# Kernel optimization log

Hardware: AMD Instinct MI355X
Metric: run time of the kernel (lower is better)

Reference implementation:

```python
import jax, jax.numpy as jnp
import numpy as np
from jax import lax

B, S, V, E, H = 64, 512, 50000, 300, 256


def _run_lstm(x, w_ih, w_hh, b_ih, b_hh, reverse):
    # x: [B,S,D]; w_ih: [4H,D]; w_hh: [4H,H]. PyTorch gate order: i,f,g,o.
    gx = jnp.einsum('bsd,gd->sbg', x, w_ih) + b_ih + b_hh  # [S,B,4H]
    Hh = w_hh.shape[1]

    def step(carry, g):
        h, c = carry
        g = g + h @ w_hh.T
        i, f, gg, o = jnp.split(g, 4, axis=-1)
        c = jax.nn.sigmoid(f) * c + jax.nn.sigmoid(i) * jnp.tanh(gg)
        h = jax.nn.sigmoid(o) * jnp.tanh(c)
        return (h, c), h

    init = (jnp.zeros((x.shape[0], Hh), x.dtype), jnp.zeros((x.shape[0], Hh), x.dtype))
    _, hs = lax.scan(step, init, gx, reverse=reverse)  # outputs aligned to input time order
    return jnp.swapaxes(hs, 0, 1)  # [B,S,H]


def _bilstm(x, wif, whf, bif, bhf, wib, whb, bib, bhb):
    fwd = _run_lstm(x, wif, whf, bif, bhf, False)
    bwd = _run_lstm(x, wib, whb, bib, bhb, True)
    return jnp.concatenate([fwd, bwd], axis=-1)  # [B,S,2H]


def setup_inputs() -> dict:
    key = jax.random.key(0)
    ks = iter(jax.random.split(key, 32))
    k = 1.0 / np.sqrt(H)
    u = lambda shape: jax.random.uniform(next(ks), shape, jnp.float32, -k, k)
    inp = {
        'input_ids': jax.random.randint(next(ks), (B, S), 0, V),
        'labels': jax.random.uniform(next(ks), (B, S), jnp.float32),
        'input_masks': jnp.ones((B, S), jnp.int64),
        'emb': jax.random.normal(next(ks), (V, E), jnp.float32) * 0.1,
    }
    # layer 0 (input E), layer 1 (input 2H); forward and backward directions
    for layer, d_in in ((0, E), (1, 2 * H)):
        for direc in ('f', 'b'):
            inp[f'w_ih_l{layer}{direc}'] = u((4 * H, d_in))
            inp[f'w_hh_l{layer}{direc}'] = u((4 * H, H))
            inp[f'b_ih_l{layer}{direc}'] = u((4 * H,))
            inp[f'b_hh_l{layer}{direc}'] = u((4 * H,))
    inp['w_lin'] = u((H,))
    inp['b_lin'] = u(())
    return inp


def reference(input_ids, labels, input_masks, emb,
              w_ih_l0f, w_hh_l0f, b_ih_l0f, b_hh_l0f,
              w_ih_l0b, w_hh_l0b, b_ih_l0b, b_hh_l0b,
              w_ih_l1f, w_hh_l1f, b_ih_l1f, b_hh_l1f,
              w_ih_l1b, w_hh_l1b, b_ih_l1b, b_hh_l1b,
              w_lin, b_lin):
    x = emb[input_ids]  # one-shot gather, replaces the double python loop: [B,S,E]
    h1 = _bilstm(x, w_ih_l0f, w_hh_l0f, b_ih_l0f, b_hh_l0f,
                 w_ih_l0b, w_hh_l0b, b_ih_l0b, b_hh_l0b)
    h2 = _bilstm(h1, w_ih_l1f, w_hh_l1f, b_ih_l1f, b_hh_l1f,
                 w_ih_l1b, w_hh_l1b, b_ih_l1b, b_hh_l1b)  # [B,S,2H]
    b, s = h2.shape[0], h2.shape[1]
    mean_dir = h2.reshape(b, s, 2, H).mean(axis=2)  # mean over directions
    scores = jax.nn.sigmoid(jnp.einsum('bsh,h->bs', mean_dir, w_lin) + b_lin)
    mask = input_masks.astype(scores.dtype)
    err = (scores - labels) ** 2 * mask
    loss = jnp.mean(jnp.sum(err, axis=1) / jnp.sum(mask, axis=1))
    return scores, loss
```

## Files before the change

### kernel.cpp

```cpp
#include <hip/hip_runtime.h>
#include <hip/hip_bf16.h>
#include <stdint.h>

#define B_  64
#define S_  512
#define E_  300
#define H_  256
#define T_  (B_*S_)
#define G4H 1024

using half8  = __attribute__((ext_vector_type(8))) _Float16;
using half4  = __attribute__((ext_vector_type(4))) _Float16;
using float4v = __attribute__((ext_vector_type(4))) float;

union H2 { _Float16 h[2]; uint32_t u; };

__device__ inline float sigm(float x) { return 1.f / (1.f + __expf(-x)); }
__device__ inline float tanhf_(float x) {
  float cx = fminf(fmaxf(x, -15.f), 15.f);
  float e = __expf(2.f * cx);
  return (e - 1.f) / (e + 1.f);
}

#define BARRIER() asm volatile("s_waitcnt lgkmcnt(0)\n\ts_barrier" ::: "memory")

__device__ inline void ld3_dev(const uint64_t* p0, const uint64_t* p1,
                               const uint64_t* p2, uint4& a, uint4& b, uint4& c) {
  asm volatile(
      "global_load_dwordx4 %0, %3, off sc0 sc1\n\t"
      "global_load_dwordx4 %1, %4, off sc0 sc1\n\t"
      "global_load_dwordx4 %2, %5, off sc0 sc1\n\t"
      "s_waitcnt vmcnt(0)"
      : "=&v"(a), "=&v"(b), "=&v"(c)
      : "v"(p0), "v"(p1), "v"(p2) : "memory");
}
__device__ inline uint4 ldx4_pin(const _Float16* p) {
  uint4 r;
  asm volatile("global_load_dwordx4 %0, %1, off\n\ts_waitcnt vmcnt(0)"
               : "=v"(r) : "v"(p));
  return r;
}

__global__ __launch_bounds__(256) void k_prep_wih(const float* __restrict__ wf,
    const float* __restrict__ wb, _Float16* __restrict__ Bt,
    int KIN, int KP, int total)
{
  int idx = blockIdx.x * 256 + threadIdx.x;
  if (idx >= total) return;
  int n = idx / KP, k = idx % KP;
  int dd = n >> 10, nn = n & 1023;
  int row = (nn & 3) * 256 + (nn >> 2);
  const float* src = dd ? wb : wf;
  Bt[idx] = (_Float16)(k < KIN ? src[row * KIN + k] : 0.f);
}

__global__ __launch_bounds__(256) void k_prep_whh(const float* __restrict__ wf,
    const float* __restrict__ wb, _Float16* __restrict__ Wr)
{
  int idx = blockIdx.x * 256 + threadIdx.x;
  int dd = idx >> 18;
  int rem = idx & 262143;
  int n = rem >> 8, k = rem & 255;
  int row = (n & 3) * 256 + (n >> 2);
  Wr[idx] = (_Float16)((dd ? wb : wf)[row * 256 + k]);
}

__global__ void k_prep_bias(const float* __restrict__ bif, const float* __restrict__ bhf,
    const float* __restrict__ bib, const float* __restrict__ bhb, float* __restrict__ bias)
{
  int n = blockIdx.x * 256 + threadIdx.x;
  int dd = n >> 10, nn = n & 1023;
  int row = (nn & 3) * 256 + (nn >> 2);
  bias[n] = dd ? (bib[row] + bhb[row]) : (bif[row] + bhf[row]);
}

__global__ __launch_bounds__(256) void k_gather(const int* __restrict__ ids,
    const float* __restrict__ emb, _Float16* __restrict__ xbf)
{
  int idx = blockIdx.x * 256 + threadIdx.x;
  int tt = idx / 40;
  int ch = idx % 40;
  int b = tt & 63, s = tt >> 6;
  int id = ids[b * S_ + s];
  const float* src = emb + (size_t)id * E_ + ch * 8;
  half8 v;
#pragma unroll
  for (int e = 0; e < 8; ++e) {
    int k = ch * 8 + e;
    v[e] = (_Float16)(k < E_ ? src[e] : 0.f);
  }
  *(half8*)(xbf + (size_t)tt * 320 + ch * 8) = v;
}

template<int K>
__global__ __launch_bounds__(256) void k_gemm(const _Float16* __restrict__ A,
    const _Float16* __restrict__ Bt, const float* __restrict__ bias,
    _Float16* __restrict__ gx)
{
  __shared__ _Float16 sA[128 * 72];
  __shared__ _Float16 sB[128 * 72];
  const int tid = threadIdx.x;
  const int t0 = blockIdx.y * 128;
  const int n0 = blockIdx.x * 128;
  const int lane = tid & 63, wid = tid >> 6;
  const int l15 = lane & 15, q = lane >> 4;
  const int wm = wid & 1, wn = wid >> 1;

  float4v acc[4][4] = {};

  for (int kt = 0; kt < K / 64; ++kt) {
    __syncthreads();
#pragma unroll
    for (int c = 0; c < 4; ++c) {
      int f = tid * 4 + c;
      int row = f >> 3, seg = f & 7;
      *(half8*)&sA[row * 72 + seg * 8] =
          *(const half8*)(A + (size_t)(t0 + row) * K + kt * 64 + seg * 8);
      *(half8*)&sB[row * 72 + seg * 8] =
          *(const half8*)(Bt + (size_t)(n0 + row) * K + kt * 64 + seg * 8);
    }
    __syncthreads();
#pragma unroll
    for (int kk = 0; kk < 2; ++kk) {
      half8 a[4], b[4];
#pragma unroll
      for (int mt = 0; mt < 4; ++mt)
        a[mt] = *(const half8*)&sA[(wm * 64 + mt * 16 + l15) * 72 + kk * 32 + q * 8];
#pragma unroll
      for (int nt = 0; nt < 4; ++nt)
        b[nt] = *(const half8*)&sB[(wn * 64 + nt * 16 + l15) * 72 + kk * 32 + q * 8];
#pragma unroll
      for (int mt = 0; mt < 4; ++mt)
#pragma unroll
        for (int nt = 0; nt < 4; ++nt)
          acc[mt][nt] = __builtin_amdgcn_mfma_f32_16x16x32_f16(a[mt], b[nt], acc[mt][nt], 0, 0, 0);
    }
  }

#pragma unroll
  for (int mt = 0; mt < 4; ++mt) {
#pragma unroll
    for (int nt = 0; nt < 4; ++nt) {
      int token = t0 + wm * 64 + mt * 16 + q * 4;
      int n = n0 + wn * 64 + nt * 16 + l15;
      float bs = bias[n];
      size_t base = (size_t)(n >> 10) * ((size_t)T_ * G4H) + (size_t)token * G4H + (n & 1023);
#pragma unroll
      for (int r = 0; r < 4; ++r)
        gx[base + (size_t)r * G4H] = (_Float16)(acc[mt][nt][r] + bs);
    }
  }
}

template<int LAYER>
__global__ __launch_bounds__(256, 1) void k_rec(const _Float16* __restrict__ gx,
    const _Float16* __restrict__ Wr, uint64_t* __restrict__ hx,
    _Float16* __restrict__ h1bf, float* __restrict__ pd2,
    const float* __restrict__ w_lin)
{
  const int tid = threadIdx.x;
  const int role = blockIdx.x;
  const int cg = role >> 2, rg = role & 3;
  const int d = cg >> 2, g = cg & 3;
  const int lane = tid & 63, wv = tid >> 6;
  const int l15 = lane & 15, q = lane >> 4;
  const int b0g = g * 16;
  const int n0g = rg * 256;

  __shared__ _Float16 hstage[16 * 288];
  __shared__ float    preS[16 * 260];

  for (int i = tid; i < 16 * 144; i += 256)
    ((uint32_t*)hstage)[i] = 0u;

  uint4 wreg[4][8];
#pragma unroll
  for (int nt = 0; nt < 4; ++nt)
#pragma unroll
    for (int kt = 0; kt < 8; ++kt)
      wreg[nt][kt] = ldx4_pin(Wr +
          (size_t)(d * G4H + n0g + wv * 64 + nt * 16 + l15) * H_ + kt * 32 + q * 8);

  const int bl = tid >> 4;
  const int jl4 = (tid & 15) * 4;
  const int bglob = b0g + bl;
  const int jg = rg * 64 + jl4;
  float wl[4];
#pragma unroll
  for (int cc = 0; cc < 4; ++cc) wl[cc] = w_lin[jg + cc];
  float creg[4] = {0.f, 0.f, 0.f, 0.f};

  uint64_t* base = hx + (size_t)cg * 2 * 2048;
  const int off2 = tid * 2;
  const int q2a = (rg + 1) & 3, q2b = (rg + 2) & 3, q2c = (rg + 3) & 3;

  half8 gxa, gxb;
  {
    const int time0 = d ? (S_ - 1) : 0;
    const _Float16* gp = gx + ((size_t)d * T_ + (size_t)time0 * B_ + bglob) * G4H
                           + n0g + (tid & 15) * 16;
    gxa = *(const half8*)(gp);
    gxb = *(const half8*)(gp + 8);
  }

  for (int t = 0; t < S_; ++t) {
    const int time = d ? (S_ - 1 - t) : t;

    if (t > 0) {
      const uint64_t* ss = base + (size_t)(t & 1) * 2048;
      const uint32_t tt = (uint32_t)t;
      uint32_t dat[6];
      unsigned pend = 0x3fu;
      for (;;) {
        uint4 A, Bv, C;
        ld3_dev(ss + q2a * 512 + off2, ss + q2b * 512 + off2,
                ss + q2c * 512 + off2, A, Bv, C);
        if ((pend & 1u)  && A.y  == tt) { dat[0] = A.x;  pend &= ~1u; }
        if ((pend & 2u)  && A.w  == tt) { dat[1] = A.z;  pend &= ~2u; }
        if ((pend & 4u)  && Bv.y == tt) { dat[2] = Bv.x; pend &= ~4u; }
        if ((pend & 8u)  && Bv.w == tt) { dat[3] = Bv.z; pend &= ~8u; }
        if ((pend & 16u) && C.y  == tt) { dat[4] = C.x;  pend &= ~16u; }
        if ((pend & 32u) && C.w  == tt) { dat[5] = C.z;  pend &= ~32u; }
        if (!pend) break;
      }
      const int sb = tid >> 4, jp = (tid & 15) * 2;
      uint2 va; va.x = dat[0]; va.y = dat[1];
      uint2 vb; vb.x = dat[2]; vb.y = dat[3];
      uint2 vc; vc.x = dat[4]; vc.y = dat[5];
      *(uint2*)&((uint32_t*)hstage)[sb * 144 + q2a * 32 + jp] = va;
      *(uint2*)&((uint32_t*)hstage)[sb * 144 + q2b * 32 + jp] = vb;
      *(uint2*)&((uint32_t*)hstage)[sb * 144 + q2c * 32 + jp] = vc;
    }
    BARRIER();

    half8 gxa_n, gxb_n;
    {
      const int tn = (t + 1 < S_) ? t + 1 : t;
      const int timen = d ? (S_ - 1 - tn) : tn;
      const _Float16* gp = gx + ((size_t)d * T_ + (size_t)timen * B_ + bglob) * G4H
                             + n0g + (tid & 15) * 16;
      gxa_n = *(const half8*)(gp);
      gxb_n = *(const half8*)(gp + 8);
    }

    float4v acc[4] = {};
#pragma unroll
    for (int kt = 0; kt < 8; ++kt) {
      half8 a = *(const half8*)&hstage[l15 * 288 + kt * 32 + q * 8];
#pragma unroll
      for (int nt = 0; nt < 4; ++nt)
        acc[nt] = __builtin_amdgcn_mfma_f32_16x16x32_f16(
            a, __builtin_bit_cast(half8, wreg[nt][kt]), acc[nt], 0, 0, 0);
    }
#pragma unroll
    for (int nt = 0; nt < 4; ++nt)
#pragma unroll
      for (int r = 0; r < 4; ++r)
        preS[(q * 4 + r) * 260 + wv * 64 + nt * 16 + l15] = acc[nt][r];
    BARRIER();

    half4 hv4;
    float partial = 0.f;
#pragma unroll
    for (int cc = 0; cc < 4; ++cc) {
      float4v p = *(const float4v*)&preS[bl * 260 + (jl4 + cc) * 4];
      float gxi = (float)(cc < 2 ? gxa[cc * 4 + 0] : gxb[(cc - 2) * 4 + 0]);
      float gxf = (float)(cc < 2 ? gxa[cc * 4 + 1] : gxb[(cc - 2) * 4 + 1]);
      float gxg = (float)(cc < 2 ? gxa[cc * 4 + 2] : gxb[(cc - 2) * 4 + 2]);
      float gxo = (float)(cc < 2 ? gxa[cc * 4 + 3] : gxb[(cc - 2) * 4 + 3]);
      float gi = p[0] + gxi, gf = p[1] + gxf, gg = p[2] + gxg, go = p[3] + gxo;
      float cv = sigm(gf) * creg[cc] + sigm(gi) * tanhf_(gg);
      float hv = sigm(go) * tanhf_(cv);
      creg[cc] = cv;
      hv4[cc] = (_Float16)hv;
      if (LAYER == 1) partial += 0.5f * hv * wl[cc];
    }

    {
      H2 p0; p0.h[0] = hv4[0]; p0.h[1] = hv4[1];
      H2 p1; p1.h[0] = hv4[2]; p1.h[1] = hv4[3];
      uint32_t tg = (uint32_t)(t + 1);
      uint64_t w0 = ((uint64_t)tg << 32) | p0.u;
      uint64_t w1 = ((uint64_t)tg << 32) | p1.u;
      uint64_t* sd = base + (size_t)((t + 1) & 1) * 2048 + rg * 512 + off2;
      __hip_atomic_store(sd + 0, w0, __ATOMIC_RELAXED, __HIP_MEMORY_SCOPE_AGENT);
      __hip_atomic_store(sd + 1, w1, __ATOMIC_RELAXED, __HIP_MEMORY_SCOPE_AGENT);
    }

    *(half4*)&hstage[bl * 288 + jg] = hv4;

    if (LAYER == 0) {
      *(half4*)(h1bf + ((size_t)time * B_ + bglob) * 512 + d * H_ + jg) = hv4;
    } else {
      partial += __shfl_xor(partial, 1);
      partial += __shfl_xor(partial, 2);
      partial += __shfl_xor(partial, 4);
      partial += __shfl_xor(partial, 8);
      if ((tid & 15) == 0)
        atomicAdd(pd2 + ((size_t)d * B_ + bglob) * S_ + time, partial);
    }

    gxa = gxa_n; gxb = gxb_n;
  }
}

__global__ __launch_bounds__(256) void k_final(const float* __restrict__ pd2,
    const float* __restrict__ labels, const int* __restrict__ masks,
    const float* __restrict__ b_lin, float* __restrict__ out)
{
  int b = blockIdx.x;
  int tid = threadIdx.x;
  float bl = b_lin[0];
  float se = 0.f, sm = 0.f;
  for (int s = tid; s < S_; s += 256) {
    float p = pd2[(size_t)b * S_ + s] + pd2[(size_t)(B_ + b) * S_ + s];
    float sc = sigm(p + bl);
    out[b * S_ + s] = sc;
    float m = (float)masks[b * S_ + s];
    float e = sc - labels[b * S_ + s];
    se += e * e * m;
    sm += m;
  }
  for (int off = 1; off < 64; off <<= 1) {
    se += __shfl_xor(se, off);
    sm += __shfl_xor(sm, off);
  }
  __shared__ float rs[4], rm[4];
  int wid = tid >> 6;
  if ((tid & 63) == 0) { rs[wid] = se; rm[wid] = sm; }
  __syncthreads();
  if (tid == 0) {
    float te = 0.f, tm = 0.f;
    for (int w = 0; w < 4; ++w) { te += rs[w]; tm += rm[w]; }
    atomicAdd(out + T_, (te / tm) * (1.f / 64.f));
  }
}

extern "C" void kernel_launch(void* const* d_in, const int* in_sizes, int n_in,
                              void* d_out, int out_size, void* d_ws, size_t ws_size,
                              hipStream_t stream)
{
  (void)in_sizes; (void)n_in; (void)out_size; (void)ws_size;
  const int*   ids    = (const int*)d_in[0];
  const float* labels = (const float*)d_in[1];
  const int*   masks  = (const int*)d_in[2];
  const float* emb    = (const float*)d_in[3];
  const float* w_ih_0f = (const float*)d_in[4];
  const float* w_hh_0f = (const float*)d_in[5];
  const float* b_ih_0f = (const float*)d_in[6];
  const float* b_hh_0f = (const float*)d_in[7];
  const float* w_ih_0b = (const float*)d_in[8];
  const float* w_hh_0b = (const float*)d_in[9];
  const float* b_ih_0b = (const float*)d_in[10];
  const float* b_hh_0b = (const float*)d_in[11];
  const float* w_ih_1f = (const float*)d_in[12];
  const float* w_hh_1f = (const float*)d_in[13];
  const float* b_ih_1f = (const float*)d_in[14];
  const float* b_hh_1f = (const float*)d_in[15];
  const float* w_ih_1b = (const float*)d_in[16];
  const float* w_hh_1b = (const float*)d_in[17];
  const float* b_ih_1b = (const float*)d_in[18];
  const float* b_hh_1b = (const float*)d_in[19];
  const float* w_lin   = (const float*)d_in[20];
  const float* b_lin   = (const float*)d_in[21];
  float* out = (float*)d_out;

  char* ws = (char*)d_ws;
  size_t off = 0;
  auto alloc = [&](size_t bytes) -> char* {
    char* p = ws + off;
    off += (bytes + 255) & ~(size_t)255;
    return p;
  };
  _Float16* xbf   = (_Float16*)alloc((size_t)T_ * 320 * 2);
  _Float16* h1bf  = (_Float16*)alloc((size_t)T_ * 512 * 2);
  _Float16* gx    = (_Float16*)alloc((size_t)2 * T_ * G4H * 2);
  _Float16* Bt0   = (_Float16*)alloc((size_t)2048 * 320 * 2);
  _Float16* Bt1   = (_Float16*)alloc((size_t)2048 * 512 * 2);
  _Float16* Wr0   = (_Float16*)alloc((size_t)2 * G4H * H_ * 2);
  _Float16* Wr1   = (_Float16*)alloc((size_t)2 * G4H * H_ * 2);
  float*    bias0 = (float*)alloc(2048 * 4);
  float*    bias1 = (float*)alloc(2048 * 4);
  uint64_t* hx0   = (uint64_t*)alloc((size_t)8 * 2 * 2048 * 8);
  uint64_t* hx1   = (uint64_t*)alloc((size_t)8 * 2 * 2048 * 8);
  float*    pd2   = (float*)alloc((size_t)2 * B_ * S_ * 4);

  k_prep_wih<<<(2048 * 320) / 256, 256, 0, stream>>>(w_ih_0f, w_ih_0b, Bt0, 300, 320, 2048 * 320);
  k_prep_wih<<<(2048 * 512) / 256, 256, 0, stream>>>(w_ih_1f, w_ih_1b, Bt1, 512, 512, 2048 * 512);
  k_prep_whh<<<524288 / 256, 256, 0, stream>>>(w_hh_0f, w_hh_0b, Wr0);
  k_prep_whh<<<524288 / 256, 256, 0, stream>>>(w_hh_1f, w_hh_1b, Wr1);
  k_prep_bias<<<8, 256, 0, stream>>>(b_ih_0f, b_hh_0f, b_ih_0b, b_hh_0b, bias0);
  k_prep_bias<<<8, 256, 0, stream>>>(b_ih_1f, b_hh_1f, b_ih_1b, b_hh_1b, bias1);
  k_gather<<<(T_ * 40) / 256, 256, 0, stream>>>(ids, emb, xbf);

  hipMemsetAsync(hx0, 0, (size_t)8 * 2 * 2048 * 8, stream);
  hipMemsetAsync(hx1, 0, (size_t)8 * 2 * 2048 * 8, stream);
  hipMemsetAsync(pd2, 0, (size_t)2 * B_ * S_ * 4, stream);
  hipMemsetAsync((char*)d_out + (size_t)T_ * 4, 0, 4, stream);

  k_gemm<320><<<dim3(16, 256), 256, 0, stream>>>(xbf, Bt0, bias0, gx);
  k_rec<0><<<32, 256, 0, stream>>>(gx, Wr0, hx0, h1bf, pd2, w_lin);

  k_gemm<512><<<dim3(16, 256), 256, 0, stream>>>(h1bf, Bt1, bias1, gx);
  k_rec<1><<<32, 256, 0, stream>>>(gx, Wr1, hx1, h1bf, pd2, w_lin);

  k_final<<<64, 256, 0, stream>>>(pd2, labels, masks, b_lin, out);
}
```

Measured before the change: 2.846 ms.

## Run each LSTM recurrence group in one workgroup, dropping cross-block global handoff

The recurrent kernel now gives each (direction, batch-group) to a single 512-thread workgroup instead of four 256-thread workgroups that exchanged hidden-state slices through tagged global-memory polling every step. W_hh is split between registers (6 of 8 tiles) and swizzled LDS (2 tiles), and h is double-buffered in LDS so each step needs one barrier. The gx pre-activation is loaded straight into the MFMA accumulators, and gates are computed directly from the accumulators, removing the preS staging. This removes the per-step inter-CU spin-wait latency, but leaves only 8 workgroups running, each doing four times the MFMA work per step with heavy register and LDS use.

```diff
diff --git a/kernel.cpp b/kernel.cpp
--- a/kernel.cpp
+++ b/kernel.cpp
@@ -13,8 +13,6 @@
 using half4  = __attribute__((ext_vector_type(4))) _Float16;
 using float4v = __attribute__((ext_vector_type(4))) float;
 
-union H2 { _Float16 h[2]; uint32_t u; };
-
 __device__ inline float sigm(float x) { return 1.f / (1.f + __expf(-x)); }
 __device__ inline float tanhf_(float x) {
   float cx = fminf(fmaxf(x, -15.f), 15.f);
@@ -24,16 +22,6 @@
 
 #define BARRIER() asm volatile("s_waitcnt lgkmcnt(0)\n\ts_barrier" ::: "memory")
 
-__device__ inline void ld3_dev(const uint64_t* p0, const uint64_t* p1,
-                               const uint64_t* p2, uint4& a, uint4& b, uint4& c) {
-  asm volatile(
-      "global_load_dwordx4 %0, %3, off sc0 sc1\n\t"
-      "global_load_dwordx4 %1, %4, off sc0 sc1\n\t"
-      "global_load_dwordx4 %2, %5, off sc0 sc1\n\t"
-      "s_waitcnt vmcnt(0)"
-      : "=&v"(a), "=&v"(b), "=&v"(c)
-      : "v"(p0), "v"(p1), "v"(p2) : "memory");
-}
 __device__ inline uint4 ldx4_pin(const _Float16* p) {
   uint4 r;
   asm volatile("global_load_dwordx4 %0, %1, off\n\ts_waitcnt vmcnt(0)"
@@ -153,154 +141,118 @@
 }
 
 template<int LAYER>
-__global__ __launch_bounds__(256, 1) void k_rec(const _Float16* __restrict__ gx,
-    const _Float16* __restrict__ Wr, uint64_t* __restrict__ hx,
-    _Float16* __restrict__ h1bf, float* __restrict__ pd2,
-    const float* __restrict__ w_lin)
-{
+__global__ __launch_bounds__(512, 2) void k_rec(const _Float16* __restrict__ gx,
+    const _Float16* __restrict__ Wr, _Float16* __restrict__ h1bf,
+    float* __restrict__ pd2, const float* __restrict__ w_lin)
+{
+  extern __shared__ char smem[];
+  _Float16* wlds = (_Float16*)smem;
+  _Float16* hst  = (_Float16*)(smem + 131072);
+  float*    wls  = (float*)(smem + 131072 + 18432);
+
   const int tid = threadIdx.x;
-  const int role = blockIdx.x;
-  const int cg = role >> 2, rg = role & 3;
+  const int cg = blockIdx.x;
   const int d = cg >> 2, g = cg & 3;
-  const int lane = tid & 63, wv = tid >> 6;
+  const int wv = tid >> 6, lane = tid & 63;
   const int l15 = lane & 15, q = lane >> 4;
   const int b0g = g * 16;
-  const int n0g = rg * 256;
-
-  __shared__ _Float16 hstage[16 * 288];
-  __shared__ float    preS[16 * 260];
-
-  for (int i = tid; i < 16 * 144; i += 256)
-    ((uint32_t*)hstage)[i] = 0u;
-
-  uint4 wreg[4][8];
-#pragma unroll
-  for (int nt = 0; nt < 4; ++nt)
+  const int bglob = b0g + l15;
+
+  if (tid < 256) wls[tid] = w_lin[tid];
+  for (int i = tid; i < 2 * 16 * 144; i += 512)
+    ((uint32_t*)hst)[i] = 0u;
+
+  uint4 wreg[6][8];
+#pragma unroll
+  for (int nt = 0; nt < 6; ++nt)
 #pragma unroll
     for (int kt = 0; kt < 8; ++kt)
       wreg[nt][kt] = ldx4_pin(Wr +
-          (size_t)(d * G4H + n0g + wv * 64 + nt * 16 + l15) * H_ + kt * 32 + q * 8);
-
-  const int bl = tid >> 4;
-  const int jl4 = (tid & 15) * 4;
-  const int bglob = b0g + bl;
-  const int jg = rg * 64 + jl4;
-  float wl[4];
-#pragma unroll
-  for (int cc = 0; cc < 4; ++cc) wl[cc] = w_lin[jg + cc];
-  float creg[4] = {0.f, 0.f, 0.f, 0.f};
-
-  uint64_t* base = hx + (size_t)cg * 2 * 2048;
-  const int off2 = tid * 2;
-  const int q2a = (rg + 1) & 3, q2b = (rg + 2) & 3, q2c = (rg + 3) & 3;
-
-  half8 gxa, gxb;
+          (size_t)(d * G4H + wv * 128 + nt * 16 + l15) * H_ + kt * 32 + q * 8);
+
+#pragma unroll
+  for (int tt = 0; tt < 2; ++tt)
+#pragma unroll
+    for (int j = 0; j < 8; ++j) {
+      int row = wv * 128 + (6 + tt) * 16 + l15;
+      uint4 w = *(const uint4*)(Wr + (size_t)(d * G4H + row) * H_ + q * 64 + j * 8);
+      int byo = (q * 128 + j * 16) ^ ((l15 & 7) << 4);
+      *(uint4*)(wlds + wv * 8192 + tt * 4096 + l15 * 256 + (byo >> 1)) = w;
+    }
+
+  float creg[8] = {};
+  uint2 gq[8];
+
   {
     const int time0 = d ? (S_ - 1) : 0;
     const _Float16* gp = gx + ((size_t)d * T_ + (size_t)time0 * B_ + bglob) * G4H
-                           + n0g + (tid & 15) * 16;
-    gxa = *(const half8*)(gp);
-    gxb = *(const half8*)(gp + 8);
-  }
+                           + wv * 128 + q * 4;
+#pragma unroll
+    for (int nt = 0; nt < 8; ++nt)
+      gq[nt] = *(const uint2*)(gp + nt * 16);
+  }
+  __syncthreads();
 
   for (int t = 0; t < S_; ++t) {
     const int time = d ? (S_ - 1 - t) : t;
-
-    if (t > 0) {
-      const uint64_t* ss = base + (size_t)(t & 1) * 2048;
-      const uint32_t tt = (uint32_t)t;
-      uint32_t dat[6];
-      unsigned pend = 0x3fu;
-      for (;;) {
-        uint4 A, Bv, C;
-        ld3_dev(ss + q2a * 512 + off2, ss + q2b * 512 + off2,
-                ss + q2c * 512 + off2, A, Bv, C);
-        if ((pend & 1u)  && A.y  == tt) { dat[0] = A.x;  pend &= ~1u; }
-        if ((pend & 2u)  && A.w  == tt) { dat[1] = A.z;  pend &= ~2u; }
-        if ((pend & 4u)  && Bv.y == tt) { dat[2] = Bv.x; pend &= ~4u; }
-        if ((pend & 8u)  && Bv.w == tt) { dat[3] = Bv.z; pend &= ~8u; }
-        if ((pend & 16u) && C.y  == tt) { dat[4] = C.x;  pend &= ~16u; }
-        if ((pend & 32u) && C.w  == tt) { dat[5] = C.z;  pend &= ~32u; }
-        if (!pend) break;
-      }
-      const int sb = tid >> 4, jp = (tid & 15) * 2;
-      uint2 va; va.x = dat[0]; va.y = dat[1];
-      uint2 vb; vb.x = dat[2]; vb.y = dat[3];
-      uint2 vc; vc.x = dat[4]; vc.y = dat[5];
-      *(uint2*)&((uint32_t*)hstage)[sb * 144 + q2a * 32 + jp] = va;
-      *(uint2*)&((uint32_t*)hstage)[sb * 144 + q2b * 32 + jp] = vb;
-      *(uint2*)&((uint32_t*)hstage)[sb * 144 + q2c * 32 + jp] = vc;
-    }
-    BARRIER();
-
-    half8 gxa_n, gxb_n;
+    const int cur = t & 1, nxt = cur ^ 1;
+
+    float4v acc[8];
+#pragma unroll
+    for (int nt = 0; nt < 8; ++nt) {
+      half4 hz = __builtin_bit_cast(half4, gq[nt]);
+      acc[nt][0] = (float)hz[0];
+      acc[nt][1] = (float)hz[1];
+      acc[nt][2] = (float)hz[2];
+      acc[nt][3] = (float)hz[3];
+    }
+
     {
       const int tn = (t + 1 < S_) ? t + 1 : t;
       const int timen = d ? (S_ - 1 - tn) : tn;
       const _Float16* gp = gx + ((size_t)d * T_ + (size_t)timen * B_ + bglob) * G4H
-                             + n0g + (tid & 15) * 16;
-      gxa_n = *(const half8*)(gp);
-      gxb_n = *(const half8*)(gp + 8);
-    }
-
-    float4v acc[4] = {};
+                             + wv * 128 + q * 4;
+#pragma unroll
+      for (int nt = 0; nt < 8; ++nt)
+        gq[nt] = *(const uint2*)(gp + nt * 16);
+    }
+
 #pragma unroll
     for (int kt = 0; kt < 8; ++kt) {
-      half8 a = *(const half8*)&hstage[l15 * 288 + kt * 32 + q * 8];
-#pragma unroll
-      for (int nt = 0; nt < 4; ++nt)
+      half8 hf = *(const half8*)(hst + cur * 4608 + l15 * 288 + kt * 32 + q * 8);
+      int byr = (kt * 64 + q * 16) ^ ((l15 & 7) << 4);
+      half8 w6 = *(const half8*)(wlds + wv * 8192 + l15 * 256 + (byr >> 1));
+      half8 w7 = *(const half8*)(wlds + wv * 8192 + 4096 + l15 * 256 + (byr >> 1));
+#pragma unroll
+      for (int nt = 0; nt < 6; ++nt)
         acc[nt] = __builtin_amdgcn_mfma_f32_16x16x32_f16(
-            a, __builtin_bit_cast(half8, wreg[nt][kt]), acc[nt], 0, 0, 0);
-    }
-#pragma unroll
-    for (int nt = 0; nt < 4; ++nt)
-#pragma unroll
-      for (int r = 0; r < 4; ++r)
-        preS[(q * 4 + r) * 260 + wv * 64 + nt * 16 + l15] = acc[nt][r];
+            __builtin_bit_cast(half8, wreg[nt][kt]), hf, acc[nt], 0, 0, 0);
+      acc[6] = __builtin_amdgcn_mfma_f32_16x16x32_f16(w6, hf, acc[6], 0, 0, 0);
+      acc[7] = __builtin_amdgcn_mfma_f32_16x16x32_f16(w7, hf, acc[7], 0, 0, 0);
+    }
+
+    float partial = 0.f;
+#pragma unroll
+    for (int nt = 0; nt < 8; ++nt) {
+      const int cell = wv * 32 + nt * 4 + q;
+      float cv = sigm(acc[nt][1]) * creg[nt] + sigm(acc[nt][0]) * tanhf_(acc[nt][2]);
+      float hv = sigm(acc[nt][3]) * tanhf_(cv);
+      creg[nt] = cv;
+      _Float16 hf16 = (_Float16)hv;
+      hst[nxt * 4608 + l15 * 288 + cell] = hf16;
+      if (LAYER == 0)
+        h1bf[((size_t)time * B_ + bglob) * 512 + d * H_ + cell] = hf16;
+      else
+        partial += 0.5f * hv * wls[cell];
+    }
+    if (LAYER == 1) {
+      partial += __shfl_xor(partial, 16);
+      partial += __shfl_xor(partial, 32);
+      if (q == 0)
+        atomicAdd(pd2 + ((size_t)d * B_ + bglob) * S_ + time, partial);
+    }
+
     BARRIER();
-
-    half4 hv4;
-    float partial = 0.f;
-#pragma unroll
-    for (int cc = 0; cc < 4; ++cc) {
-      float4v p = *(const float4v*)&preS[bl * 260 + (jl4 + cc) * 4];
-      float gxi = (float)(cc < 2 ? gxa[cc * 4 + 0] : gxb[(cc - 2) * 4 + 0]);
-      float gxf = (float)(cc < 2 ? gxa[cc * 4 + 1] : gxb[(cc - 2) * 4 + 1]);
-      float gxg = (float)(cc < 2 ? gxa[cc * 4 + 2] : gxb[(cc - 2) * 4 + 2]);
-      float gxo = (float)(cc < 2 ? gxa[cc * 4 + 3] : gxb[(cc - 2) * 4 + 3]);
-      float gi = p[0] + gxi, gf = p[1] + gxf, gg = p[2] + gxg, go = p[3] + gxo;
-      float cv = sigm(gf) * creg[cc] + sigm(gi) * tanhf_(gg);
-      float hv = sigm(go) * tanhf_(cv);
-      creg[cc] = cv;
-      hv4[cc] = (_Float16)hv;
-      if (LAYER == 1) partial += 0.5f * hv * wl[cc];
-    }
-
-    {
-      H2 p0; p0.h[0] = hv4[0]; p0.h[1] = hv4[1];
-      H2 p1; p1.h[0] = hv4[2]; p1.h[1] = hv4[3];
-      uint32_t tg = (uint32_t)(t + 1);
-      uint64_t w0 = ((uint64_t)tg << 32) | p0.u;
-      uint64_t w1 = ((uint64_t)tg << 32) | p1.u;
-      uint64_t* sd = base + (size_t)((t + 1) & 1) * 2048 + rg * 512 + off2;
-      __hip_atomic_store(sd + 0, w0, __ATOMIC_RELAXED, __HIP_MEMORY_SCOPE_AGENT);
-      __hip_atomic_store(sd + 1, w1, __ATOMIC_RELAXED, __HIP_MEMORY_SCOPE_AGENT);
-    }
-
-    *(half4*)&hstage[bl * 288 + jg] = hv4;
-
-    if (LAYER == 0) {
-      *(half4*)(h1bf + ((size_t)time * B_ + bglob) * 512 + d * H_ + jg) = hv4;
-    } else {
-      partial += __shfl_xor(partial, 1);
-      partial += __shfl_xor(partial, 2);
-      partial += __shfl_xor(partial, 4);
-      partial += __shfl_xor(partial, 8);
-      if ((tid & 15) == 0)
-        atomicAdd(pd2 + ((size_t)d * B_ + bglob) * S_ + time, partial);
-    }
-
-    gxa = gxa_n; gxb = gxb_n;
   }
 }
 
@@ -381,9 +333,12 @@
   _Float16* Wr1   = (_Float16*)alloc((size_t)2 * G4H * H_ * 2);
   float*    bias0 = (float*)alloc(2048 * 4);
   float*    bias1 = (float*)alloc(2048 * 4);
-  uint64_t* hx0   = (uint64_t*)alloc((size_t)8 * 2 * 2048 * 8);
-  uint64_t* hx1   = (uint64_t*)alloc((size_t)8 * 2 * 2048 * 8);
   float*    pd2   = (float*)alloc((size_t)2 * B_ * S_ * 4);
+
+  (void)hipFuncSetAttribute(reinterpret_cast<const void*>(&k_rec<0>),
+                            hipFuncAttributeMaxDynamicSharedMemorySize, 150528);
+  (void)hipFuncSetAttribute(reinterpret_cast<const void*>(&k_rec<1>),
+                            hipFuncAttributeMaxDynamicSharedMemorySize, 150528);
 
   k_prep_wih<<<(2048 * 320) / 256, 256, 0, stream>>>(w_ih_0f, w_ih_0b, Bt0, 300, 320, 2048 * 320);
   k_prep_wih<<<(2048 * 512) / 256, 256, 0, stream>>>(w_ih_1f, w_ih_1b, Bt1, 512, 512, 2048 * 512);
@@ -393,16 +348,14 @@
   k_prep_bias<<<8, 256, 0, stream>>>(b_ih_1f, b_hh_1f, b_ih_1b, b_hh_1b, bias1);
   k_gather<<<(T_ * 40) / 256, 256, 0, stream>>>(ids, emb, xbf);
 
-  hipMemsetAsync(hx0, 0, (size_t)8 * 2 * 2048 * 8, stream);
-  hipMemsetAsync(hx1, 0, (size_t)8 * 2 * 2048 * 8, stream);
   hipMemsetAsync(pd2, 0, (size_t)2 * B_ * S_ * 4, stream);
   hipMemsetAsync((char*)d_out + (size_t)T_ * 4, 0, 4, stream);
 
   k_gemm<320><<<dim3(16, 256), 256, 0, stream>>>(xbf, Bt0, bias0, gx);
-  k_rec<0><<<32, 256, 0, stream>>>(gx, Wr0, hx0, h1bf, pd2, w_lin);
+  k_rec<0><<<8, 512, 150528, stream>>>(gx, Wr0, h1bf, pd2, w_lin);
 
   k_gemm<512><<<dim3(16, 256), 256, 0, stream>>>(h1bf, Bt1, bias1, gx);
-  k_rec<1><<<32, 256, 0, stream>>>(gx, Wr1, hx1, h1bf, pd2, w_lin);
+  k_rec<1><<<8, 512, 150528, stream>>>(gx, Wr1, h1bf, pd2, w_lin);
 
   k_final<<<64, 256, 0, stream>>>(pd2, labels, masks, b_lin, out);
 }
```

Measured after the change: 5.567 ms. +95.6%, slower.

## Compute LSTM gates in MFMA registers, removing preactivation LDS round-trip and barrier

Applied to the files above, without the earlier changes.

The recurrent kernel permutes the weight rows held in registers and swaps the MFMA operands, so each lane's accumulator holds the i,f,g,o preactivations for its own hidden units. The gate nonlinearities can then run directly from registers, which drops the preS shared-memory staging and one block barrier per timestep. The accumulator is seeded from the precomputed input projection, the h staging buffer is double-buffered, and w_lin moves to shared memory. The handoff layout between blocks changes to match the new lane mapping, so any mismatch in the permutation would corrupt results.

```diff
diff --git a/kernel.cpp b/kernel.cpp
--- a/kernel.cpp
+++ b/kernel.cpp
@@ -158,53 +158,50 @@
     _Float16* __restrict__ h1bf, float* __restrict__ pd2,
     const float* __restrict__ w_lin)
 {
+  __shared__ _Float16 hst[2][16 * 264];
+  __shared__ float    wls[256];
+
   const int tid = threadIdx.x;
   const int role = blockIdx.x;
   const int cg = role >> 2, rg = role & 3;
   const int d = cg >> 2, g = cg & 3;
   const int lane = tid & 63, wv = tid >> 6;
   const int l15 = lane & 15, q = lane >> 4;
-  const int b0g = g * 16;
-  const int n0g = rg * 256;
-
-  __shared__ _Float16 hstage[16 * 288];
-  __shared__ float    preS[16 * 260];
-
-  for (int i = tid; i < 16 * 144; i += 256)
-    ((uint32_t*)hstage)[i] = 0u;
+  const int bglob = g * 16 + l15;
+
+  if (tid < 256) wls[tid] = w_lin[tid];
+  for (int i = tid; i < 2 * 16 * 132; i += 256)
+    ((uint32_t*)&hst[0][0])[i] = 0u;
 
   uint4 wreg[4][8];
 #pragma unroll
   for (int nt = 0; nt < 4; ++nt)
 #pragma unroll
-    for (int kt = 0; kt < 8; ++kt)
-      wreg[nt][kt] = ldx4_pin(Wr +
-          (size_t)(d * G4H + n0g + wv * 64 + nt * 16 + l15) * H_ + kt * 32 + q * 8);
-
-  const int bl = tid >> 4;
-  const int jl4 = (tid & 15) * 4;
-  const int bglob = b0g + bl;
-  const int jg = rg * 64 + jl4;
-  float wl[4];
-#pragma unroll
-  for (int cc = 0; cc < 4; ++cc) wl[cc] = w_lin[jg + cc];
+    for (int kt = 0; kt < 8; ++kt) {
+      int row = rg * 256 + wv * 64 + (l15 >> 2) * 16 + nt * 4 + (l15 & 3);
+      wreg[nt][kt] = ldx4_pin(Wr + (size_t)(d * G4H + row) * H_ + kt * 32 + q * 8);
+    }
+
   float creg[4] = {0.f, 0.f, 0.f, 0.f};
 
   uint64_t* base = hx + (size_t)cg * 2 * 2048;
   const int off2 = tid * 2;
   const int q2a = (rg + 1) & 3, q2b = (rg + 2) & 3, q2c = (rg + 3) & 3;
-
-  half8 gxa, gxb;
+  const int jloc = rg * 64 + wv * 16 + q * 4;
+
+  uint4 gqa, gqb;
   {
     const int time0 = d ? (S_ - 1) : 0;
     const _Float16* gp = gx + ((size_t)d * T_ + (size_t)time0 * B_ + bglob) * G4H
-                           + n0g + (tid & 15) * 16;
-    gxa = *(const half8*)(gp);
-    gxb = *(const half8*)(gp + 8);
-  }
+                           + rg * 256 + wv * 64 + q * 16;
+    gqa = *(const uint4*)(gp);
+    gqb = *(const uint4*)(gp + 8);
+  }
+  __syncthreads();
 
   for (int t = 0; t < S_; ++t) {
     const int time = d ? (S_ - 1 - t) : t;
+    const int cur = t & 1, nxt = cur ^ 1;
 
     if (t > 0) {
       const uint64_t* ss = base + (size_t)(t & 1) * 2048;
@@ -224,56 +221,57 @@
         if (!pend) break;
       }
       const int sb = tid >> 4, jp = (tid & 15) * 2;
+      uint32_t* hc = (uint32_t*)&hst[cur][0];
       uint2 va; va.x = dat[0]; va.y = dat[1];
       uint2 vb; vb.x = dat[2]; vb.y = dat[3];
       uint2 vc; vc.x = dat[4]; vc.y = dat[5];
-      *(uint2*)&((uint32_t*)hstage)[sb * 144 + q2a * 32 + jp] = va;
-      *(uint2*)&((uint32_t*)hstage)[sb * 144 + q2b * 32 + jp] = vb;
-      *(uint2*)&((uint32_t*)hstage)[sb * 144 + q2c * 32 + jp] = vc;
+      *(uint2*)&hc[sb * 132 + q2a * 32 + jp] = va;
+      *(uint2*)&hc[sb * 132 + q2b * 32 + jp] = vb;
+      *(uint2*)&hc[sb * 132 + q2c * 32 + jp] = vc;
     }
     BARRIER();
 
-    half8 gxa_n, gxb_n;
+    uint4 gqa_n, gqb_n;
     {
       const int tn = (t + 1 < S_) ? t + 1 : t;
       const int timen = d ? (S_ - 1 - tn) : tn;
       const _Float16* gp = gx + ((size_t)d * T_ + (size_t)timen * B_ + bglob) * G4H
-                             + n0g + (tid & 15) * 16;
-      gxa_n = *(const half8*)(gp);
-      gxb_n = *(const half8*)(gp + 8);
-    }
-
-    float4v acc[4] = {};
+                             + rg * 256 + wv * 64 + q * 16;
+      gqa_n = *(const uint4*)(gp);
+      gqb_n = *(const uint4*)(gp + 8);
+    }
+
+    float4v acc[4];
+    {
+      half8 ga = __builtin_bit_cast(half8, gqa);
+      half8 gb = __builtin_bit_cast(half8, gqb);
+#pragma unroll
+      for (int r = 0; r < 4; ++r) {
+        acc[0][r] = (float)ga[r];
+        acc[1][r] = (float)ga[4 + r];
+        acc[2][r] = (float)gb[r];
+        acc[3][r] = (float)gb[4 + r];
+      }
+    }
+
 #pragma unroll
     for (int kt = 0; kt < 8; ++kt) {
-      half8 a = *(const half8*)&hstage[l15 * 288 + kt * 32 + q * 8];
+      half8 hf = *(const half8*)&hst[cur][l15 * 264 + kt * 32 + q * 8];
 #pragma unroll
       for (int nt = 0; nt < 4; ++nt)
         acc[nt] = __builtin_amdgcn_mfma_f32_16x16x32_f16(
-            a, __builtin_bit_cast(half8, wreg[nt][kt]), acc[nt], 0, 0, 0);
-    }
-#pragma unroll
-    for (int nt = 0; nt < 4; ++nt)
-#pragma unroll
-      for (int r = 0; r < 4; ++r)
-        preS[(q * 4 + r) * 260 + wv * 64 + nt * 16 + l15] = acc[nt][r];
-    BARRIER();
+            __builtin_bit_cast(half8, wreg[nt][kt]), hf, acc[nt], 0, 0, 0);
+    }
 
     half4 hv4;
     float partial = 0.f;
 #pragma unroll
-    for (int cc = 0; cc < 4; ++cc) {
-      float4v p = *(const float4v*)&preS[bl * 260 + (jl4 + cc) * 4];
-      float gxi = (float)(cc < 2 ? gxa[cc * 4 + 0] : gxb[(cc - 2) * 4 + 0]);
-      float gxf = (float)(cc < 2 ? gxa[cc * 4 + 1] : gxb[(cc - 2) * 4 + 1]);
-      float gxg = (float)(cc < 2 ? gxa[cc * 4 + 2] : gxb[(cc - 2) * 4 + 2]);
-      float gxo = (float)(cc < 2 ? gxa[cc * 4 + 3] : gxb[(cc - 2) * 4 + 3]);
-      float gi = p[0] + gxi, gf = p[1] + gxf, gg = p[2] + gxg, go = p[3] + gxo;
-      float cv = sigm(gf) * creg[cc] + sigm(gi) * tanhf_(gg);
-      float hv = sigm(go) * tanhf_(cv);
-      creg[cc] = cv;
-      hv4[cc] = (_Float16)hv;
-      if (LAYER == 1) partial += 0.5f * hv * wl[cc];
+    for (int nt = 0; nt < 4; ++nt) {
+      float cv = sigm(acc[nt][1]) * creg[nt] + sigm(acc[nt][0]) * tanhf_(acc[nt][2]);
+      float hv = sigm(acc[nt][3]) * tanhf_(cv);
+      creg[nt] = cv;
+      hv4[nt] = (_Float16)hv;
+      if (LAYER == 1) partial += 0.5f * hv * wls[jloc + nt];
     }
 
     {
@@ -282,25 +280,24 @@
       uint32_t tg = (uint32_t)(t + 1);
       uint64_t w0 = ((uint64_t)tg << 32) | p0.u;
       uint64_t w1 = ((uint64_t)tg << 32) | p1.u;
-      uint64_t* sd = base + (size_t)((t + 1) & 1) * 2048 + rg * 512 + off2;
+      uint64_t* sd = base + (size_t)((t + 1) & 1) * 2048 + rg * 512
+                   + l15 * 32 + wv * 8 + q * 2;
       __hip_atomic_store(sd + 0, w0, __ATOMIC_RELAXED, __HIP_MEMORY_SCOPE_AGENT);
       __hip_atomic_store(sd + 1, w1, __ATOMIC_RELAXED, __HIP_MEMORY_SCOPE_AGENT);
     }
 
-    *(half4*)&hstage[bl * 288 + jg] = hv4;
+    *(half4*)&hst[nxt][l15 * 264 + jloc] = hv4;
 
     if (LAYER == 0) {
-      *(half4*)(h1bf + ((size_t)time * B_ + bglob) * 512 + d * H_ + jg) = hv4;
+      *(half4*)(h1bf + ((size_t)time * B_ + bglob) * 512 + d * H_ + jloc) = hv4;
     } else {
-      partial += __shfl_xor(partial, 1);
-      partial += __shfl_xor(partial, 2);
-      partial += __shfl_xor(partial, 4);
-      partial += __shfl_xor(partial, 8);
-      if ((tid & 15) == 0)
+      partial += __shfl_xor(partial, 16);
+      partial += __shfl_xor(partial, 32);
+      if (q == 0)
         atomicAdd(pd2 + ((size_t)d * B_ + bglob) * S_ + time, partial);
     }
 
-    gxa = gxa_n; gxb = gxb_n;
+    gqa = gqa_n; gqb = gqb_n;
   }
 }
 
```

Result: no change. 2.856 ms (+0.3%).
